# Performance work log

Measured on AMD Instinct MI355X. Metric: run time of the kernel, lower is better.

## Reference

```python
import jax, jax.numpy as jnp
import numpy as np

B, S, V, E, H, M, CS, U = 1, 2048, 50257, 512, 768, 256, 64, 2048


def setup_inputs() -> dict:
    key = jax.random.key(0)
    ks = jax.random.split(key, 16)
    s = 0.02
    p = {}
    p["input_ids"] = jax.random.randint(ks[0], (B, S), 0, V)
    p["untied_token_ids"] = jax.random.randint(ks[1], (U,), 0, V)
    p["emb"] = jax.random.normal(ks[2], (V, E)) * s
    p["w_ih"] = jax.random.normal(ks[3], (3 * H, E)) * s
    p["w_hh"] = jax.random.normal(ks[4], (3 * H, H)) * s
    p["b_ih"] = jnp.zeros((3 * H,))
    p["b_hh"] = jnp.zeros((3 * H,))
    p["Wq"] = jax.random.normal(ks[5], (M, H)) * s
    p["bq"] = jnp.zeros((M,))
    p["Wk"] = jax.random.normal(ks[6], (M, H)) * s
    p["bk"] = jnp.zeros((M,))
    p["Whf"] = jax.random.normal(ks[7], (4 * E, H)) * s
    p["bhf"] = jnp.zeros((4 * E,))
    p["Whp"] = jax.random.normal(ks[8], (E, 4 * E)) * s
    p["bhp"] = jnp.zeros((E,))
    p["Wcv"] = jax.random.normal(ks[9], (E, H)) * s
    p["bcv"] = jnp.zeros((E,))
    p["Wph"] = jax.random.normal(ks[10], (U, E)) * s
    p["bph"] = jnp.zeros((U,))
    p["out_bias"] = jnp.zeros((V,))
    return p


def gru(x, w_ih, w_hh, b_ih, b_hh):
    # x: [B, S, E] -> states [B, S, H]; PyTorch GRU gate order (r, z, n)
    Hh = w_hh.shape[1]

    def step(h, xt):
        gx = xt @ w_ih.T + b_ih
        gh = h @ w_hh.T + b_hh
        xr, xz, xn = jnp.split(gx, 3, axis=-1)
        hr, hz, hn = jnp.split(gh, 3, axis=-1)
        r = jax.nn.sigmoid(xr + hr)
        z = jax.nn.sigmoid(xz + hz)
        n = jnp.tanh(xn + r * hn)
        h = (1.0 - z) * n + z * h
        return h, h

    h0 = jnp.zeros((x.shape[0], Hh), x.dtype)
    _, hs = jax.lax.scan(step, h0, jnp.swapaxes(x, 0, 1))
    return jnp.swapaxes(hs, 0, 1)


def reference(input_ids, untied_token_ids, emb, w_ih, w_hh, b_ih, b_hh, Wq, bq, Wk, bk, Whf, bhf, Whp, bhp, Wcv, bcv, Wph, bph, out_bias):
    x = emb[input_ids]                                  # [B,S,E]
    states = gru(x, w_ih, w_hh, b_ih, b_hh)             # [B,S,H] (dropout=0, eval)
    head = jnp.square(jax.nn.relu(states @ Whf.T + bhf))  # [B,S,4E]
    base_feat = head @ Whp.T + bhp                      # [B,S,E]
    base_logits = base_feat @ emb.T + out_bias          # [B,S,V]

    nc = S // CS  # S == max_length, divisible by chunk_size -> pad_len = 0
    chunked = states.reshape(B, nc, CS, H).mean(axis=2)  # [B,nc,H]
    qk = states @ Wq.T + bq                              # [B,S,M]
    mk = chunked @ Wk.T + bk                             # [B,nc,M]
    scores = jnp.einsum('bsm,bcm->bsc', qk, mk) / jnp.sqrt(jnp.asarray(M, qk.dtype))

    chunk_ends = jnp.minimum(jnp.arange(nc) * CS + (CS - 1), S - 1)
    mask = chunk_ends[None, None, :] < jnp.arange(S)[None, :, None]  # [1,S,nc]
    neg = jnp.finfo(scores.dtype).min
    scores = jnp.where(mask, scores, neg)
    attn = jax.nn.softmax(scores, axis=-1) * mask
    attn = attn / jnp.clip(attn.sum(axis=-1, keepdims=True), 1e-6)

    base_partial = base_feat @ Wph.T + bph               # [B,S,U]
    chunk_partial = (chunked @ Wcv.T + bcv) @ Wph.T + bph  # [B,nc,U]
    mem_partial = jnp.einsum('bsc,bcu->bsu', attn, chunk_partial)
    total_partial = base_partial + mem_partial           # [B,S,U]

    # scatter_add partial logits into full-vocab logits (duplicates accumulate)
    return base_logits.at[:, :, untied_token_ids].add(total_partial)
```

## Files before the change

### kernel.cpp

```cpp
#include <hip/hip_runtime.h>
#include <hip/hip_bf16.h>
#include <math.h>

#define SEQ   2048
#define VOC   50257
#define EMB   512
#define HID   768
#define G3    2304
#define MDIM  256
#define CSZ   64
#define NCHUNK 32
#define UDIM  2048
#define E4    2048

#define G_GRU 48
#define CANARY 0xFFFFFFFFu

typedef uint32_t u32x4  __attribute__((ext_vector_type(4)));
typedef float    f32x4  __attribute__((ext_vector_type(4)));
typedef short    s16x8  __attribute__((ext_vector_type(8)));
typedef __bf16   bf16x8 __attribute__((ext_vector_type(8)));

__global__ __launch_bounds__(256) void embed_kernel(const int* __restrict__ ids,
                                                    const float* __restrict__ emb,
                                                    float* __restrict__ X) {
    int s = blockIdx.x;
    int id = ids[s];
    const float* src = &emb[(size_t)id * EMB];
    float* dst = &X[(size_t)s * EMB];
    for (int i = threadIdx.x; i < EMB; i += 256) dst[i] = src[i];
}

template<int EPI>
__global__ __launch_bounds__(256) void gemm_nt(const float* __restrict__ A,
                                               const float* __restrict__ B,
                                               const float* __restrict__ bias,
                                               float* __restrict__ C,
                                               int M, int N, int K) {
    __shared__ float As[16][132];
    __shared__ float Bs[16][132];
    const int tid = threadIdx.x;
    const int tx = tid & 15;
    const int ty = tid >> 4;
    const int m0 = blockIdx.y * 128;
    const int n0 = blockIdx.x * 128;

    float acc[8][8];
    #pragma unroll
    for (int i = 0; i < 8; i++)
        #pragma unroll
        for (int j = 0; j < 8; j++) acc[i][j] = 0.f;

    for (int k0 = 0; k0 < K; k0 += 16) {
        #pragma unroll
        for (int i = 0; i < 2; i++) {
            int idx = tid * 2 + i;
            int r   = idx >> 2;
            int c4  = idx & 3;
            float4 av = {0.f, 0.f, 0.f, 0.f};
            float4 bv = {0.f, 0.f, 0.f, 0.f};
            int ar = m0 + r;
            if (ar < M) av = *reinterpret_cast<const float4*>(&A[(size_t)ar * K + k0 + c4 * 4]);
            int br = n0 + r;
            if (br < N) bv = *reinterpret_cast<const float4*>(&B[(size_t)br * K + k0 + c4 * 4]);
            As[c4 * 4 + 0][r] = av.x; As[c4 * 4 + 1][r] = av.y;
            As[c4 * 4 + 2][r] = av.z; As[c4 * 4 + 3][r] = av.w;
            Bs[c4 * 4 + 0][r] = bv.x; Bs[c4 * 4 + 1][r] = bv.y;
            Bs[c4 * 4 + 2][r] = bv.z; Bs[c4 * 4 + 3][r] = bv.w;
        }
        __syncthreads();
        #pragma unroll
        for (int k = 0; k < 16; k++) {
            float4 a0 = *reinterpret_cast<const float4*>(&As[k][ty * 4]);
            float4 a1 = *reinterpret_cast<const float4*>(&As[k][64 + ty * 4]);
            float4 b0 = *reinterpret_cast<const float4*>(&Bs[k][tx * 4]);
            float4 b1 = *reinterpret_cast<const float4*>(&Bs[k][64 + tx * 4]);
            float a[8] = {a0.x, a0.y, a0.z, a0.w, a1.x, a1.y, a1.z, a1.w};
            float b[8] = {b0.x, b0.y, b0.z, b0.w, b1.x, b1.y, b1.z, b1.w};
            #pragma unroll
            for (int i = 0; i < 8; i++)
                #pragma unroll
                for (int j = 0; j < 8; j++)
                    acc[i][j] = fmaf(a[i], b[j], acc[i][j]);
        }
        __syncthreads();
    }

    #pragma unroll
    for (int i = 0; i < 8; i++) {
        int r = m0 + ((i < 4) ? (ty * 4 + i) : (64 + ty * 4 + (i - 4)));
        if (r >= M) continue;
        #pragma unroll
        for (int j = 0; j < 8; j++) {
            int c = n0 + ((j < 4) ? (tx * 4 + j) : (64 + tx * 4 + (j - 4)));
            if (c >= N) continue;
            float v = acc[i][j] + bias[c];
            if (EPI == 1) { v = fmaxf(v, 0.f); v = v * v; }
            C[(size_t)r * N + c] = v;
        }
    }
}

__global__ __launch_bounds__(256) void gemm_bf16_logits(const float* __restrict__ A,
                                                        const float* __restrict__ B,
                                                        const float* __restrict__ bias,
                                                        float* __restrict__ C,
                                                        int M, int N, int K) {
    constexpr int LDT = 40;
    __shared__ __bf16 As[128 * LDT];
    __shared__ __bf16 Bs[128 * LDT];
    const int tid  = threadIdx.x;
    const int lane = tid & 63;
    const int wave = tid >> 6;
    const int wm = wave >> 1;
    const int wn = wave & 1;
    const int m0 = blockIdx.y * 128;
    const int n0 = blockIdx.x * 128;
    const int l15 = lane & 15;
    const int l4  = lane >> 4;

    f32x4 acc[4][4];
    #pragma unroll
    for (int i = 0; i < 4; i++)
        #pragma unroll
        for (int j = 0; j < 4; j++) acc[i][j] = (f32x4){0.f, 0.f, 0.f, 0.f};

    const int r  = tid >> 1;
    const int hf = tid & 1;

    for (int k0 = 0; k0 < K; k0 += 32) {
        const float* ap = &A[(size_t)(m0 + r) * K + k0 + hf * 16];
        float4 a0 = *reinterpret_cast<const float4*>(ap);
        float4 a1 = *reinterpret_cast<const float4*>(ap + 4);
        float4 a2 = *reinterpret_cast<const float4*>(ap + 8);
        float4 a3 = *reinterpret_cast<const float4*>(ap + 12);
        int bn = n0 + r;
        float4 b0 = {0,0,0,0}, b1 = {0,0,0,0}, b2 = {0,0,0,0}, b3 = {0,0,0,0};
        if (bn < N) {
            const float* bp = &B[(size_t)bn * K + k0 + hf * 16];
            b0 = *reinterpret_cast<const float4*>(bp);
            b1 = *reinterpret_cast<const float4*>(bp + 4);
            b2 = *reinterpret_cast<const float4*>(bp + 8);
            b3 = *reinterpret_cast<const float4*>(bp + 12);
        }
        __syncthreads();
        {
            __bf16* da = &As[r * LDT + hf * 16];
            bf16x8 w0, w1;
            w0[0]=(__bf16)a0.x; w0[1]=(__bf16)a0.y; w0[2]=(__bf16)a0.z; w0[3]=(__bf16)a0.w;
            w0[4]=(__bf16)a1.x; w0[5]=(__bf16)a1.y; w0[6]=(__bf16)a1.z; w0[7]=(__bf16)a1.w;
            w1[0]=(__bf16)a2.x; w1[1]=(__bf16)a2.y; w1[2]=(__bf16)a2.z; w1[3]=(__bf16)a2.w;
            w1[4]=(__bf16)a3.x; w1[5]=(__bf16)a3.y; w1[6]=(__bf16)a3.z; w1[7]=(__bf16)a3.w;
            *reinterpret_cast<bf16x8*>(da)     = w0;
            *reinterpret_cast<bf16x8*>(da + 8) = w1;
            __bf16* db = &Bs[r * LDT + hf * 16];
            bf16x8 v0, v1;
            v0[0]=(__bf16)b0.x; v0[1]=(__bf16)b0.y; v0[2]=(__bf16)b0.z; v0[3]=(__bf16)b0.w;
            v0[4]=(__bf16)b1.x; v0[5]=(__bf16)b1.y; v0[6]=(__bf16)b1.z; v0[7]=(__bf16)b1.w;
            v1[0]=(__bf16)b2.x; v1[1]=(__bf16)b2.y; v1[2]=(__bf16)b2.z; v1[3]=(__bf16)b2.w;
            v1[4]=(__bf16)b3.x; v1[5]=(__bf16)b3.y; v1[6]=(__bf16)b3.z; v1[7]=(__bf16)b3.w;
            *reinterpret_cast<bf16x8*>(db)     = v0;
            *reinterpret_cast<bf16x8*>(db + 8) = v1;
        }
        __syncthreads();

        s16x8 af[4], bf[4];
        #pragma unroll
        for (int i = 0; i < 4; i++)
            af[i] = *reinterpret_cast<const s16x8*>(&As[(wm * 64 + i * 16 + l15) * LDT + l4 * 8]);
        #pragma unroll
        for (int j = 0; j < 4; j++)
            bf[j] = *reinterpret_cast<const s16x8*>(&Bs[(wn * 64 + j * 16 + l15) * LDT + l4 * 8]);
        #pragma unroll
        for (int i = 0; i < 4; i++)
            #pragma unroll
            for (int j = 0; j < 4; j++)
                acc[i][j] = __builtin_amdgcn_mfma_f32_16x16x32_bf16(af[i], bf[j], acc[i][j], 0, 0, 0);
    }

    #pragma unroll
    for (int j = 0; j < 4; j++) {
        int col = n0 + wn * 64 + j * 16 + l15;
        if (col >= N) continue;
        float bv = bias[col];
        #pragma unroll
        for (int i = 0; i < 4; i++) {
            int row = m0 + wm * 64 + i * 16 + l4 * 4;
            #pragma unroll
            for (int q = 0; q < 4; q++)
                C[(size_t)(row + q) * N + col] = acc[i][j][q] + bv;
        }
    }
}

__device__ __forceinline__ float fast_sigmoid(float x) {
    x = fminf(fmaxf(x, -30.f), 30.f);
    return __builtin_amdgcn_rcpf(1.f + __expf(-x));
}
__device__ __forceinline__ float fast_tanh(float x) {
    x = fminf(fmaxf(x, -15.f), 15.f);
    float e = __expf(2.f * x);
    return (e - 1.f) * __builtin_amdgcn_rcpf(e + 1.f);
}

__global__ __launch_bounds__(256, 1) void gru_kernel(const float* __restrict__ GX,
                                                     const float* __restrict__ Whh,
                                                     const float* __restrict__ bhh,
                                                     float* __restrict__ states) {
    __shared__ float h_s[HID];
    const int tid  = threadIdx.x;
    const int g    = blockIdx.x;
    const int tx   = tid & 15;
    const int ty   = tid >> 4;
    const int gu   = g * 16 + ty;
    const int wave = tid >> 6;
    const int lane = tid & 63;

    float4 W4[3][12];
    #pragma unroll
    for (int p = 0; p < 3; p++) {
        const float* wr = &Whh[(size_t)(p * HID + gu) * HID + 4 * tx];
        #pragma unroll
        for (int j = 0; j < 12; j++)
            W4[p][j] = *reinterpret_cast<const float4*>(&wr[64 * j]);
    }
    float bh[3];
    #pragma unroll
    for (int p = 0; p < 3; p++) bh[p] = bhh[p * HID + gu];

    float hv  = 0.f;
    float gx0 = GX[0 * HID + gu];
    float gx1 = GX[1 * HID + gu];
    float gx2 = GX[2 * HID + gu];

    for (int t = 0; t < SEQ; t++) {
        float ngx0 = 0.f, ngx1 = 0.f, ngx2 = 0.f;
        if (t + 1 < SEQ) {
            const float* gp = &GX[(size_t)(t + 1) * G3];
            ngx0 = gp[0 * HID + gu];
            ngx1 = gp[1 * HID + gu];
            ngx2 = gp[2 * HID + gu];
        }

        float4 h4[12];
        if (t > 0) {
            if (tid < 192) {
                const float* pp = states + (size_t)(t - 1) * HID + tid * 4;
                u32x4 q;
                float s;
                do {
                    asm volatile(
                        "global_load_dwordx4 %0, %1, off sc0 sc1\n\t"
                        "s_waitcnt vmcnt(0)"
                        : "=&v"(q) : "v"(pp) : "memory");
                    f32x4 f = __builtin_bit_cast(f32x4, q);
                    s = f[0] + f[1] + f[2] + f[3];
                } while (s != s);
                *reinterpret_cast<u32x4*>(&h_s[tid * 4]) = q;
            }
            __syncthreads();
            #pragma unroll
            for (int j = 0; j < 12; j++)
                h4[j] = *reinterpret_cast<const float4*>(&h_s[4 * tx + 64 * j]);
        } else {
            #pragma unroll
            for (int j = 0; j < 12; j++) h4[j] = make_float4(0.f, 0.f, 0.f, 0.f);
        }

        float accp[3];
        #pragma unroll
        for (int p = 0; p < 3; p++) {
            float a = 0.f;
            #pragma unroll
            for (int j = 0; j < 12; j++) {
                a = fmaf(W4[p][j].x, h4[j].x, a);
                a = fmaf(W4[p][j].y, h4[j].y, a);
                a = fmaf(W4[p][j].z, h4[j].z, a);
                a = fmaf(W4[p][j].w, h4[j].w, a);
            }
            accp[p] = a;
        }
        #pragma unroll
        for (int p = 0; p < 3; p++) {
            accp[p] += __shfl_xor(accp[p], 1);
            accp[p] += __shfl_xor(accp[p], 2);
            accp[p] += __shfl_xor(accp[p], 4);
            accp[p] += __shfl_xor(accp[p], 8);
        }

        float r = fast_sigmoid(gx0 + accp[0] + bh[0]);
        float z = fast_sigmoid(gx1 + accp[1] + bh[1]);
        float n = fast_tanh(gx2 + r * (accp[2] + bh[2]));
        hv = (1.f - z) * n + z * hv;

        float v0 = __shfl(hv, 0);
        float v1 = __shfl(hv, 16);
        float v2 = __shfl(hv, 32);
        float v3 = __shfl(hv, 48);
        if (lane == 0) {
            f32x4 pv = {v0, v1, v2, v3};
            float* dp = states + (size_t)t * HID + g * 16 + wave * 4;
            asm volatile(
                "global_store_dwordx4 %0, %1, off sc0 sc1"
                :: "v"(dp), "v"(pv) : "memory");
        }
        gx0 = ngx0; gx1 = ngx1; gx2 = ngx2;
    }
}

__global__ __launch_bounds__(256) void chunkmean_kernel(const float* __restrict__ states,
                                                        float* __restrict__ chunked) {
    int c = blockIdx.x;
    for (int e = threadIdx.x; e < HID; e += 256) {
        float s = 0.f;
        #pragma unroll 8
        for (int i = 0; i < CSZ; i++)
            s += states[(size_t)(c * CSZ + i) * HID + e];
        chunked[c * HID + e] = s * (1.f / 64.f);
    }
}

__global__ void attn_kernel(const float* __restrict__ qk,
                            const float* __restrict__ mk,
                            float* __restrict__ attn) {
    int s = blockIdx.x;
    int lane = threadIdx.x;
    int c = lane & 31;
    int h = lane >> 5;
    const float* q = &qk[(size_t)s * MDIM];
    const float* m = &mk[(size_t)c * MDIM];
    float sc = 0.f;
    for (int k = h; k < MDIM; k += 2) sc = fmaf(q[k], m[k], sc);
    sc += __shfl_xor(sc, 32);
    sc *= (1.0f / 16.0f);
    bool allowed = (CSZ * c + (CSZ - 1)) < s;
    float v = allowed ? sc : -3.4e38f;
    float mx = v;
    #pragma unroll
    for (int d = 16; d >= 1; d >>= 1) mx = fmaxf(mx, __shfl_xor(mx, d));
    float e = (allowed && mx > -1e37f) ? expf(sc - mx) : 0.f;
    float sm = e;
    #pragma unroll
    for (int d = 16; d >= 1; d >>= 1) sm += __shfl_xor(sm, d);
    float a = (sm > 0.f) ? e / sm : 0.f;
    if (lane < 32) attn[(size_t)s * NCHUNK + c] = a;
}

__global__ __launch_bounds__(256) void total_scatter_kernel(const float* __restrict__ bp,
                                                            const float* __restrict__ cp,
                                                            const float* __restrict__ attn,
                                                            const int* __restrict__ uids,
                                                            float* __restrict__ out) {
    int s = blockIdx.x;
    __shared__ float a_s[NCHUNK];
    if (threadIdx.x < NCHUNK) a_s[threadIdx.x] = attn[(size_t)s * NCHUNK + threadIdx.x];
    __syncthreads();
    for (int u = threadIdx.x; u < UDIM; u += 256) {
        float t = bp[(size_t)s * UDIM + u];
        #pragma unroll 8
        for (int c = 0; c < NCHUNK; c++)
            t = fmaf(a_s[c], cp[(size_t)c * UDIM + u], t);
        atomicAdd(&out[(size_t)s * VOC + uids[u]], t);
    }
}

extern "C" void kernel_launch(void* const* d_in, const int* in_sizes, int n_in,
                              void* d_out, int out_size, void* d_ws, size_t ws_size,
                              hipStream_t stream) {
    const int*   ids   = (const int*)d_in[0];
    const int*   uids  = (const int*)d_in[1];
    const float* emb   = (const float*)d_in[2];
    const float* w_ih  = (const float*)d_in[3];
    const float* w_hh  = (const float*)d_in[4];
    const float* b_ih  = (const float*)d_in[5];
    const float* b_hh  = (const float*)d_in[6];
    const float* Wq    = (const float*)d_in[7];
    const float* bq    = (const float*)d_in[8];
    const float* Wk    = (const float*)d_in[9];
    const float* bk    = (const float*)d_in[10];
    const float* Whf   = (const float*)d_in[11];
    const float* bhf   = (const float*)d_in[12];
    const float* Whp   = (const float*)d_in[13];
    const float* bhp   = (const float*)d_in[14];
    const float* Wcv   = (const float*)d_in[15];
    const float* bcv   = (const float*)d_in[16];
    const float* Wph   = (const float*)d_in[17];
    const float* bph   = (const float*)d_in[18];
    const float* obias = (const float*)d_in[19];
    float* out = (float*)d_out;
    float* wsf = (float*)d_ws;

    size_t off = 0;
    float* X      = wsf + off; off += (size_t)SEQ * EMB;
    float* GX     = wsf + off; off += (size_t)SEQ * G3;
    float* states = wsf + off; off += (size_t)SEQ * HID;
    float* head   = wsf + off; off += (size_t)SEQ * E4;
    float* bfeat  = wsf + off; off += (size_t)SEQ * EMB;
    float* chunk  = wsf + off; off += (size_t)NCHUNK * HID;
    float* qk     = wsf + off; off += (size_t)SEQ * MDIM;
    float* mk     = wsf + off; off += (size_t)NCHUNK * MDIM;
    float* cv     = wsf + off; off += (size_t)NCHUNK * EMB;
    float* cp     = wsf + off; off += (size_t)NCHUNK * UDIM;
    float* bp     = wsf + off; off += (size_t)SEQ * UDIM;
    float* attn   = wsf + off; off += (size_t)SEQ * NCHUNK;

    embed_kernel<<<SEQ, 256, 0, stream>>>(ids, emb, X);
    hipMemsetAsync(states, 0xFF, (size_t)SEQ * HID * sizeof(float), stream);
    gemm_nt<0><<<dim3(G3 / 128, SEQ / 128), 256, 0, stream>>>(X, w_ih, b_ih, GX, SEQ, G3, EMB);
    gru_kernel<<<G_GRU, 256, 0, stream>>>(GX, w_hh, b_hh, states);
    chunkmean_kernel<<<NCHUNK, 256, 0, stream>>>(states, chunk);
    gemm_nt<0><<<dim3(MDIM / 128, SEQ / 128), 256, 0, stream>>>(states, Wq, bq, qk, SEQ, MDIM, HID);
    gemm_nt<0><<<dim3(MDIM / 128, 1), 256, 0, stream>>>(chunk, Wk, bk, mk, NCHUNK, MDIM, HID);
    gemm_nt<1><<<dim3(E4 / 128, SEQ / 128), 256, 0, stream>>>(states, Whf, bhf, head, SEQ, E4, HID);
    gemm_nt<0><<<dim3(EMB / 128, SEQ / 128), 256, 0, stream>>>(head, Whp, bhp, bfeat, SEQ, EMB, E4);
    gemm_nt<0><<<dim3(EMB / 128, 1), 256, 0, stream>>>(chunk, Wcv, bcv, cv, NCHUNK, EMB, HID);
    gemm_nt<0><<<dim3(UDIM / 128, 1), 256, 0, stream>>>(cv, Wph, bph, cp, NCHUNK, UDIM, EMB);
    gemm_nt<0><<<dim3(UDIM / 128, SEQ / 128), 256, 0, stream>>>(bfeat, Wph, bph, bp, SEQ, UDIM, EMB);
    gemm_bf16_logits<<<dim3((VOC + 127) / 128, SEQ / 128), 256, 0, stream>>>(bfeat, emb, obias, out, SEQ, VOC, EMB);
    attn_kernel<<<SEQ, 64, 0, stream>>>(qk, mk, attn);
    total_scatter_kernel<<<SEQ, 256, 0, stream>>>(bp, cp, attn, uids, out);
}
```

Measured before the change: 5.744 ms.

## Pre-convert weights and activations to bf16 and use MFMA GEMMs

Adds a float-to-bf16 conversion kernel and a bf16 MFMA GEMM that takes pre-converted operands. The embedding table, w_ih, Whp and Wph are converted each call, and head and bfeat are converted after they are produced. The input projection, the head down-projection, the untied partial GEMM and the logits GEMM then use MFMA with bf16 inputs, replacing the scalar fp32 FMA tiling and the in-loop conversion in the logits kernel. This costs extra conversion passes, notably the full 50257x512 embedding table on every call, and lowers precision on several GEMMs. The path is taken only when the workspace is large enough; otherwise the old sequence runs.

```diff
diff --git a/kernel.cpp b/kernel.cpp
--- a/kernel.cpp
+++ b/kernel.cpp
@@ -21,6 +21,19 @@
 typedef short    s16x8  __attribute__((ext_vector_type(8)));
 typedef __bf16   bf16x8 __attribute__((ext_vector_type(8)));
 
+__global__ __launch_bounds__(256) void cvt_f32_bf16(const float* __restrict__ src,
+                                                    __bf16* __restrict__ dst, int n8) {
+    int stride = gridDim.x * 256;
+    for (int i = blockIdx.x * 256 + threadIdx.x; i < n8; i += stride) {
+        const float4* s = reinterpret_cast<const float4*>(src + (size_t)i * 8);
+        float4 a = s[0], b = s[1];
+        bf16x8 o;
+        o[0]=(__bf16)a.x; o[1]=(__bf16)a.y; o[2]=(__bf16)a.z; o[3]=(__bf16)a.w;
+        o[4]=(__bf16)b.x; o[5]=(__bf16)b.y; o[6]=(__bf16)b.z; o[7]=(__bf16)b.w;
+        *reinterpret_cast<bf16x8*>(dst + (size_t)i * 8) = o;
+    }
+}
+
 __global__ __launch_bounds__(256) void embed_kernel(const int* __restrict__ ids,
                                                     const float* __restrict__ emb,
                                                     float* __restrict__ X) {
@@ -29,6 +42,17 @@
     const float* src = &emb[(size_t)id * EMB];
     float* dst = &X[(size_t)s * EMB];
     for (int i = threadIdx.x; i < EMB; i += 256) dst[i] = src[i];
+}
+
+__global__ __launch_bounds__(64) void embed16_kernel(const int* __restrict__ ids,
+                                                     const __bf16* __restrict__ emb16,
+                                                     __bf16* __restrict__ X16) {
+    int s = blockIdx.x;
+    int id = ids[s];
+    const bf16x8* src = reinterpret_cast<const bf16x8*>(emb16 + (size_t)id * EMB);
+    bf16x8* dst = reinterpret_cast<bf16x8*>(X16 + (size_t)s * EMB);
+    int i = threadIdx.x;
+    dst[i] = src[i];
 }
 
 template<int EPI>
@@ -97,6 +121,86 @@
             float v = acc[i][j] + bias[c];
             if (EPI == 1) { v = fmaxf(v, 0.f); v = v * v; }
             C[(size_t)r * N + c] = v;
+        }
+    }
+}
+
+template<int EPI>
+__global__ __launch_bounds__(256) void gemm_bt16(const __bf16* __restrict__ A,
+                                                 const __bf16* __restrict__ B,
+                                                 const float* __restrict__ bias,
+                                                 float* __restrict__ C,
+                                                 int M, int N, int K) {
+    constexpr int LDT = 40;
+    __shared__ __bf16 As[128 * LDT];
+    __shared__ __bf16 Bs[128 * LDT];
+    const int tid  = threadIdx.x;
+    const int lane = tid & 63;
+    const int wave = tid >> 6;
+    const int wm = wave >> 1;
+    const int wn = wave & 1;
+    const int m0 = blockIdx.y * 128;
+    const int n0 = blockIdx.x * 128;
+    const int l15 = lane & 15;
+    const int l4  = lane >> 4;
+
+    f32x4 acc[4][4];
+    #pragma unroll
+    for (int i = 0; i < 4; i++)
+        #pragma unroll
+        for (int j = 0; j < 4; j++) acc[i][j] = (f32x4){0.f, 0.f, 0.f, 0.f};
+
+    const int r  = tid >> 1;
+    const int hf = tid & 1;
+
+    for (int k0 = 0; k0 < K; k0 += 32) {
+        const __bf16* ap = &A[(size_t)(m0 + r) * K + k0 + hf * 16];
+        s16x8 av0 = *reinterpret_cast<const s16x8*>(ap);
+        s16x8 av1 = *reinterpret_cast<const s16x8*>(ap + 8);
+        s16x8 bv0, bv1;
+        #pragma unroll
+        for (int q = 0; q < 8; q++) { bv0[q] = 0; bv1[q] = 0; }
+        int bn = n0 + r;
+        if (bn < N) {
+            const __bf16* bp = &B[(size_t)bn * K + k0 + hf * 16];
+            bv0 = *reinterpret_cast<const s16x8*>(bp);
+            bv1 = *reinterpret_cast<const s16x8*>(bp + 8);
+        }
+        __syncthreads();
+        *reinterpret_cast<s16x8*>(&As[r * LDT + hf * 16])     = av0;
+        *reinterpret_cast<s16x8*>(&As[r * LDT + hf * 16 + 8]) = av1;
+        *reinterpret_cast<s16x8*>(&Bs[r * LDT + hf * 16])     = bv0;
+        *reinterpret_cast<s16x8*>(&Bs[r * LDT + hf * 16 + 8]) = bv1;
+        __syncthreads();
+
+        s16x8 af[4], bf[4];
+        #pragma unroll
+        for (int i = 0; i < 4; i++)
+            af[i] = *reinterpret_cast<const s16x8*>(&As[(wm * 64 + i * 16 + l15) * LDT + l4 * 8]);
+        #pragma unroll
+        for (int j = 0; j < 4; j++)
+            bf[j] = *reinterpret_cast<const s16x8*>(&Bs[(wn * 64 + j * 16 + l15) * LDT + l4 * 8]);
+        #pragma unroll
+        for (int i = 0; i < 4; i++)
+            #pragma unroll
+            for (int j = 0; j < 4; j++)
+                acc[i][j] = __builtin_amdgcn_mfma_f32_16x16x32_bf16(af[i], bf[j], acc[i][j], 0, 0, 0);
+    }
+
+    #pragma unroll
+    for (int j = 0; j < 4; j++) {
+        int col = n0 + wn * 64 + j * 16 + l15;
+        if (col >= N) continue;
+        float bv = bias[col];
+        #pragma unroll
+        for (int i = 0; i < 4; i++) {
+            int row = m0 + wm * 64 + i * 16 + l4 * 4;
+            #pragma unroll
+            for (int q = 0; q < 4; q++) {
+                float v = acc[i][j][q] + bv;
+                if (EPI == 1) { v = fmaxf(v, 0.f); v = v * v; }
+                C[(size_t)(row + q) * N + col] = v;
+            }
         }
     }
 }
@@ -362,6 +466,11 @@
             t = fmaf(a_s[c], cp[(size_t)c * UDIM + u], t);
         atomicAdd(&out[(size_t)s * VOC + uids[u]], t);
     }
+}
+
+static inline int cvt_grid(int n8) {
+    int g = (n8 + 255) / 256;
+    return g > 2048 ? 2048 : g;
 }
 
 extern "C" void kernel_launch(void* const* d_in, const int* in_sizes, int n_in,
@@ -391,7 +500,6 @@
     float* wsf = (float*)d_ws;
 
     size_t off = 0;
-    float* X      = wsf + off; off += (size_t)SEQ * EMB;
     float* GX     = wsf + off; off += (size_t)SEQ * G3;
     float* states = wsf + off; off += (size_t)SEQ * HID;
     float* head   = wsf + off; off += (size_t)SEQ * E4;
@@ -403,20 +511,55 @@
     float* cp     = wsf + off; off += (size_t)NCHUNK * UDIM;
     float* bp     = wsf + off; off += (size_t)SEQ * UDIM;
     float* attn   = wsf + off; off += (size_t)SEQ * NCHUNK;
-
-    embed_kernel<<<SEQ, 256, 0, stream>>>(ids, emb, X);
-    hipMemsetAsync(states, 0xFF, (size_t)SEQ * HID * sizeof(float), stream);
-    gemm_nt<0><<<dim3(G3 / 128, SEQ / 128), 256, 0, stream>>>(X, w_ih, b_ih, GX, SEQ, G3, EMB);
-    gru_kernel<<<G_GRU, 256, 0, stream>>>(GX, w_hh, b_hh, states);
-    chunkmean_kernel<<<NCHUNK, 256, 0, stream>>>(states, chunk);
-    gemm_nt<0><<<dim3(MDIM / 128, SEQ / 128), 256, 0, stream>>>(states, Wq, bq, qk, SEQ, MDIM, HID);
-    gemm_nt<0><<<dim3(MDIM / 128, 1), 256, 0, stream>>>(chunk, Wk, bk, mk, NCHUNK, MDIM, HID);
-    gemm_nt<1><<<dim3(E4 / 128, SEQ / 128), 256, 0, stream>>>(states, Whf, bhf, head, SEQ, E4, HID);
-    gemm_nt<0><<<dim3(EMB / 128, SEQ / 128), 256, 0, stream>>>(head, Whp, bhp, bfeat, SEQ, EMB, E4);
-    gemm_nt<0><<<dim3(EMB / 128, 1), 256, 0, stream>>>(chunk, Wcv, bcv, cv, NCHUNK, EMB, HID);
-    gemm_nt<0><<<dim3(UDIM / 128, 1), 256, 0, stream>>>(cv, Wph, bph, cp, NCHUNK, UDIM, EMB);
-    gemm_nt<0><<<dim3(UDIM / 128, SEQ / 128), 256, 0, stream>>>(bfeat, Wph, bph, bp, SEQ, UDIM, EMB);
-    gemm_bf16_logits<<<dim3((VOC + 127) / 128, SEQ / 128), 256, 0, stream>>>(bfeat, emb, obias, out, SEQ, VOC, EMB);
-    attn_kernel<<<SEQ, 64, 0, stream>>>(qk, mk, attn);
-    total_scatter_kernel<<<SEQ, 256, 0, stream>>>(bp, cp, attn, uids, out);
-}
+    size_t common_off = off;
+
+    __bf16* X16     = (__bf16*)(wsf + off); off += (size_t)SEQ * EMB / 2;
+    __bf16* emb16   = (__bf16*)(wsf + off); off += (size_t)VOC * EMB / 2;
+    __bf16* wih16   = (__bf16*)(wsf + off); off += (size_t)G3 * EMB / 2;
+    __bf16* Whp16   = (__bf16*)(wsf + off); off += (size_t)EMB * E4 / 2;
+    __bf16* Wph16   = (__bf16*)(wsf + off); off += (size_t)UDIM * EMB / 2;
+    __bf16* head16  = (__bf16*)(wsf + off); off += (size_t)SEQ * E4 / 2;
+    __bf16* bfeat16 = (__bf16*)(wsf + off); off += (size_t)SEQ * EMB / 2;
+    const bool big = ws_size >= off * sizeof(float);
+
+    if (big) {
+        cvt_f32_bf16<<<cvt_grid(VOC * EMB / 8), 256, 0, stream>>>(emb, emb16, VOC * EMB / 8);
+        cvt_f32_bf16<<<cvt_grid(G3 * EMB / 8), 256, 0, stream>>>(w_ih, wih16, G3 * EMB / 8);
+        cvt_f32_bf16<<<cvt_grid(EMB * E4 / 8), 256, 0, stream>>>(Whp, Whp16, EMB * E4 / 8);
+        cvt_f32_bf16<<<cvt_grid(UDIM * EMB / 8), 256, 0, stream>>>(Wph, Wph16, UDIM * EMB / 8);
+        embed16_kernel<<<SEQ, 64, 0, stream>>>(ids, emb16, X16);
+        hipMemsetAsync(states, 0xFF, (size_t)SEQ * HID * sizeof(float), stream);
+        gemm_bt16<0><<<dim3(G3 / 128, SEQ / 128), 256, 0, stream>>>(X16, wih16, b_ih, GX, SEQ, G3, EMB);
+        gru_kernel<<<G_GRU, 256, 0, stream>>>(GX, w_hh, b_hh, states);
+        chunkmean_kernel<<<NCHUNK, 256, 0, stream>>>(states, chunk);
+        gemm_nt<0><<<dim3(MDIM / 128, SEQ / 128), 256, 0, stream>>>(states, Wq, bq, qk, SEQ, MDIM, HID);
+        gemm_nt<0><<<dim3(MDIM / 128, 1), 256, 0, stream>>>(chunk, Wk, bk, mk, NCHUNK, MDIM, HID);
+        gemm_nt<1><<<dim3(E4 / 128, SEQ / 128), 256, 0, stream>>>(states, Whf, bhf, head, SEQ, E4, HID);
+        cvt_f32_bf16<<<cvt_grid(SEQ * E4 / 8), 256, 0, stream>>>(head, head16, SEQ * E4 / 8);
+        gemm_bt16<0><<<dim3(EMB / 128, SEQ / 128), 256, 0, stream>>>(head16, Whp16, bhp, bfeat, SEQ, EMB, E4);
+        cvt_f32_bf16<<<cvt_grid(SEQ * EMB / 8), 256, 0, stream>>>(bfeat, bfeat16, SEQ * EMB / 8);
+        gemm_nt<0><<<dim3(EMB / 128, 1), 256, 0, stream>>>(chunk, Wcv, bcv, cv, NCHUNK, EMB, HID);
+        gemm_nt<0><<<dim3(UDIM / 128, 1), 256, 0, stream>>>(cv, Wph, bph, cp, NCHUNK, UDIM, EMB);
+        gemm_bt16<0><<<dim3(UDIM / 128, SEQ / 128), 256, 0, stream>>>(bfeat16, Wph16, bph, bp, SEQ, UDIM, EMB);
+        gemm_bt16<0><<<dim3((VOC + 127) / 128, SEQ / 128), 256, 0, stream>>>(bfeat16, emb16, obias, out, SEQ, VOC, EMB);
+        attn_kernel<<<SEQ, 64, 0, stream>>>(qk, mk, attn);
+        total_scatter_kernel<<<SEQ, 256, 0, stream>>>(bp, cp, attn, uids, out);
+    } else {
+        float* X = wsf + common_off;
+        embed_kernel<<<SEQ, 256, 0, stream>>>(ids, emb, X);
+        hipMemsetAsync(states, 0xFF, (size_t)SEQ * HID * sizeof(float), stream);
+        gemm_nt<0><<<dim3(G3 / 128, SEQ / 128), 256, 0, stream>>>(X, w_ih, b_ih, GX, SEQ, G3, EMB);
+        gru_kernel<<<G_GRU, 256, 0, stream>>>(GX, w_hh, b_hh, states);
+        chunkmean_kernel<<<NCHUNK, 256, 0, stream>>>(states, chunk);
+        gemm_nt<0><<<dim3(MDIM / 128, SEQ / 128), 256, 0, stream>>>(states, Wq, bq, qk, SEQ, MDIM, HID);
+        gemm_nt<0><<<dim3(MDIM / 128, 1), 256, 0, stream>>>(chunk, Wk, bk, mk, NCHUNK, MDIM, HID);
+        gemm_nt<1><<<dim3(E4 / 128, SEQ / 128), 256, 0, stream>>>(states, Whf, bhf, head, SEQ, E4, HID);
+        gemm_nt<0><<<dim3(EMB / 128, SEQ / 128), 256, 0, stream>>>(head, Whp, bhp, bfeat, SEQ, EMB, E4);
+        gemm_nt<0><<<dim3(EMB / 128, 1), 256, 0, stream>>>(chunk, Wcv, bcv, cv, NCHUNK, EMB, HID);
+        gemm_nt<0><<<dim3(UDIM / 128, 1), 256, 0, stream>>>(cv, Wph, bph, cp, NCHUNK, UDIM, EMB);
+        gemm_nt<0><<<dim3(UDIM / 128, SEQ / 128), 256, 0, stream>>>(bfeat, Wph, bph, bp, SEQ, UDIM, EMB);
+        gemm_bf16_logits<<<dim3((VOC + 127) / 128, SEQ / 128), 256, 0, stream>>>(bfeat, emb, obias, out, SEQ, VOC, EMB);
+        attn_kernel<<<SEQ, 64, 0, stream>>>(qk, mk, attn);
+        total_scatter_kernel<<<SEQ, 256, 0, stream>>>(bp, cp, attn, uids, out);
+    }
+}
```

New measurement: 5.172 ms. -10.0%, faster.
